# Kernel optimization log

Hardware: AMD Instinct MI355X
Metric: run time of the kernel (lower is better)

## Reference

```python
import jax, jax.numpy as jnp
import numpy as np

MP1, NX, P, HT, HE = 524288, 32768, 128, 128, 64


def setup_inputs() -> dict:
    key = jax.random.key(0)
    ks = jax.random.split(key, 12)
    w = lambda k, shape, fan_in: jax.random.normal(k, shape, jnp.float32) / np.sqrt(fan_in).astype(np.float32)
    a = jax.random.normal(ks[0], (MP1,), jnp.float32)
    x = jax.random.uniform(ks[1], (NX,), jnp.float32)
    t = jax.random.uniform(ks[2], (), jnp.float32)
    # DeepONet-style operator net: branch Linear(Mp1 -> p), trunk MLP (x,t) -> p
    Wb = w(ks[3], (P, MP1), MP1); bb = jnp.zeros((P,), jnp.float32)
    Wt1 = w(ks[4], (HT, 2), 2); bt1 = jnp.zeros((HT,), jnp.float32)
    Wt2 = w(ks[5], (HT, HT), HT); bt2 = jnp.zeros((HT,), jnp.float32)
    Wt3 = w(ks[6], (P, HT), HT); bt3 = jnp.zeros((P,), jnp.float32)
    # EnergyNet F(y,z): tiny smooth MLP R^2 -> R (needs 3rd-order derivatives)
    We1 = w(ks[7], (HE, 2), 2); be1 = jnp.zeros((HE,), jnp.float32)
    We2 = w(ks[8], (HE, HE), HE); be2 = jnp.zeros((HE,), jnp.float32)
    We3 = w(ks[9], (1, HE), HE); be3 = jnp.zeros((1,), jnp.float32)
    return dict(a=a, x=x, t=t, Wb=Wb, bb=bb, Wt1=Wt1, bt1=bt1, Wt2=Wt2, bt2=bt2,
                Wt3=Wt3, bt3=bt3, We1=We1, be1=be1, We2=We2, be2=be2, We3=We3, be3=be3)


def reference(a, x, t, Wb, bb, Wt1, bt1, Wt2, bt2, Wt3, bt3, We1, be1, We2, be2, We3, be3):
    # branch encoding of the input function a: (P,)
    b = Wb @ a + bb

    def u_fn(xi):  # scalar x -> scalar u(x, t)
        h = jnp.tanh(Wt1 @ jnp.stack([xi, t]) + bt1)
        h = jnp.tanh(Wt2 @ h + bt2)
        return jnp.dot(b, Wt3 @ h + bt3)

    def F(y, z):  # EnergyNet: scalar (y, z) -> scalar
        h = jnp.tanh(We1 @ jnp.stack([y, z]) + be1)
        h = jnp.tanh(We2 @ h + be2)
        return (We3 @ h + be3)[0]

    # u and its spatial derivatives, vmapped over the Nx grid points
    u = jax.vmap(u_fn)(x)
    u_x = jax.vmap(jax.grad(u_fn))(x)
    u_xx = jax.vmap(jax.grad(jax.grad(u_fn)))(x)
    u_xxx = jax.vmap(jax.grad(jax.grad(jax.grad(u_fn))))(x)

    # all needed partials of F(y, z), exactly as in the original module
    F_y = jax.grad(F)
    F_yz = jax.vmap(jax.grad(F_y, 1))(u, u_x)
    F_yy, F_yyz = jax.vmap(jax.value_and_grad(jax.grad(F_y), 1))(u, u_x)
    F_zz, (F_yzz, F_zzz) = jax.vmap(jax.value_and_grad(jax.grad(jax.grad(F, 1), 1), (0, 1)))(u, u_x)

    F_yx = F_yy * u_x + F_yz * u_xx
    F_zxx = (F_yz * u_xx + F_zz * u_xxx + F_yyz * u_x ** 2
             + 2.0 * F_yzz * u_x * u_xx + F_zzz * u_xx ** 2)
    return (-F_yx + F_zxx).reshape(x.shape[0])
```

## Files before the change

kernel.cpp:

```cpp
#include <hip/hip_runtime.h>
#include <cmath>

#define MP1 524288
#define NXP 32768

typedef float vfloat4 __attribute__((ext_vector_type(4)));

#define PART_   0
#define CVEC_   4096
#define UCONST_ 4224
#define WT2T_   8192
#define WE2T_   24576

__device__ __forceinline__ float tanh_fast(float x) {
    x = fminf(20.f, fmaxf(-20.f, x));
    float t = exp2f(x * 2.8853900817779268f);
    return (t - 1.f) * __builtin_amdgcn_rcpf(t + 1.f);
}

__global__ __launch_bounds__(256) void gemv_k(const float* __restrict__ Wb,
                                              const float* __restrict__ a,
                                              float* __restrict__ ws) {
    const int row = blockIdx.x;
    const int chunk = blockIdx.y;
    const int t = threadIdx.x;
    size_t base = (size_t)row * MP1 + (size_t)chunk * 16384;
    const vfloat4* W4 = (const vfloat4*)(Wb + base);
    const float4* A4 = (const float4*)(a + (size_t)chunk * 16384);
    float sum = 0.0f;
#pragma unroll
    for (int it = 0; it < 16; ++it) {
        vfloat4 w = __builtin_nontemporal_load(&W4[t + it * 256]);
        float4 av = A4[t + it * 256];
        sum += w[0] * av.x + w[1] * av.y + w[2] * av.z + w[3] * av.w;
    }
#pragma unroll
    for (int off = 32; off > 0; off >>= 1) sum += __shfl_down(sum, off, 64);
    __shared__ float red[4];
    int wid = t >> 6;
    if ((t & 63) == 0) red[wid] = sum;
    __syncthreads();
    if (t == 0) ws[PART_ + row * 32 + chunk] = red[0] + red[1] + red[2] + red[3];
}

__global__ __launch_bounds__(256) void prep_k(const float* __restrict__ bb,
                                              const float* __restrict__ Wt2,
                                              const float* __restrict__ We2,
                                              const float* __restrict__ Wt3,
                                              const float* __restrict__ bt3,
                                              float* __restrict__ ws) {
    const int tid = threadIdx.x;
    if (blockIdx.x == 0) {
        __shared__ float sh[128];
        __shared__ float red[2];
        if (tid < 128) {
            float b = bb[tid];
            const float* part = ws + PART_ + tid * 32;
#pragma unroll
            for (int c = 0; c < 32; ++c) b += part[c];
            sh[tid] = b;
        }
        __syncthreads();
        if (tid < 128) {
            float cv = 0.f;
            for (int j = 0; j < 128; ++j) cv = fmaf(sh[j], Wt3[j * 128 + tid], cv);
            ws[CVEC_ + tid] = cv;
            float p = sh[tid] * bt3[tid];
#pragma unroll
            for (int off = 32; off > 0; off >>= 1) p += __shfl_down(p, off, 64);
            if ((tid & 63) == 0) red[tid >> 6] = p;
        }
        __syncthreads();
        if (tid == 0) ws[UCONST_] = red[0] + red[1];
    } else {
        int idx = (blockIdx.x - 1) * 256 + tid;
        int j = idx >> 7, k = idx & 127;
        ws[WT2T_ + k * 128 + j] = Wt2[idx];
        if (idx < 4096) {
            int m = idx >> 6, i2 = idx & 63;
            ws[WE2T_ + i2 * 64 + m] = We2[idx];
        }
    }
}

#define SW_WT1 0
#define SW_BT1 256
#define SW_BT2 384
#define SW_CVEC 512
#define SW_WE1X 640
#define SW_BE1 1152
#define SW_BE2 1216
#define SW_WE3 1280
#define UREDP 1344
#define H1V_ 1600
#define FREDP (H1V_ + 4096)
#define SCR_ 9792
#define LDSF 13888

__global__ __launch_bounds__(512, 4) void point_k(const float* __restrict__ x,
                                                  const float* __restrict__ tptr,
                                                  const float* __restrict__ Wt1,
                                                  const float* __restrict__ bt1,
                                                  const float* __restrict__ bt2,
                                                  const float* __restrict__ We1,
                                                  const float* __restrict__ be1,
                                                  const float* __restrict__ be2,
                                                  const float* __restrict__ We3,
                                                  const float* __restrict__ ws,
                                                  float* __restrict__ out) {
    __shared__ __align__(16) float lds[LDSF];
    const int tid = threadIdx.x;
    const int p = tid & 63;
    const int slice = __builtin_amdgcn_readfirstlane(tid >> 6);
    const int i = blockIdx.x * 64 + p;
    const float xi = x[i];
    const float tt = tptr[0];
    const float u_const = ws[UCONST_];

    if (tid < 256) lds[SW_WT1 + tid] = Wt1[tid];
    else if (tid < 384) lds[SW_BT1 + tid - 256] = bt1[tid - 256];
    else lds[SW_BT2 + tid - 384] = bt2[tid - 384];
    if (tid < 128) lds[SW_CVEC + tid] = ws[CVEC_ + tid];
    else if (tid < 192) lds[SW_BE1 + tid - 128] = be1[tid - 128];
    else if (tid < 256) lds[SW_BE2 + tid - 192] = be2[tid - 192];
    else if (tid < 320) lds[SW_WE3 + tid - 256] = We3[tid - 256];
    else if (tid < 384) {
        int ii = tid - 320;
        float w0 = We1[2 * ii], w1 = We1[2 * ii + 1];
        float w00 = w0 * w0, w01 = w0 * w1, w11 = w1 * w1;
        float* X = lds + SW_WE1X + ii * 8;
        X[0] = w0; X[1] = w1; X[2] = w00; X[3] = w01; X[4] = w11;
        X[5] = w00 * w1; X[6] = w01 * w1; X[7] = w11 * w1;
    }
    __syncthreads();

#pragma unroll
    for (int q = 0; q < 16; ++q) {
        int k = slice * 16 + q;
        float z = fmaf(lds[SW_WT1 + 2 * k], xi,
                       fmaf(lds[SW_WT1 + 2 * k + 1], tt, lds[SW_BT1 + k]));
        lds[H1V_ + k * 64 + p] = tanh_fast(z);
    }

    float a0[16], a1[16], a2[16], a3[16];
#pragma unroll
    for (int jj = 0; jj < 16; ++jj) { a0[jj] = 0.f; a1[jj] = 0.f; a2[jj] = 0.f; a3[jj] = 0.f; }
    for (int c = 0; c < 4; ++c) {
        __syncthreads();
        {
            const float4* src = (const float4*)(ws + WT2T_ + c * 4096);
            float4* dst = (float4*)(lds + SCR_);
            dst[tid] = src[tid];
            dst[tid + 512] = src[tid + 512];
        }
        __syncthreads();
#pragma unroll 1
        for (int kl = 0; kl < 32; ++kl) {
            int k = c * 32 + kl;
            float v = lds[H1V_ + k * 64 + p];
            float w = lds[SW_WT1 + 2 * k];
            float s = fmaf(-v, v, 1.f);
            float t2 = v * s;
            float m = fmaf(-3.f, s, 2.f);
            float sm = s * m;
            float w2 = w * w, w3 = w2 * w;
            float d1 = s * w;
            float d2 = t2 * w2;
            float d3 = sm * w3;
            const float4* wr = (const float4*)(lds + SCR_ + kl * 128 + slice * 16);
            float4 wv0 = wr[0], wv1 = wr[1], wv2 = wr[2], wv3 = wr[3];
            const float wf[16] = {wv0.x, wv0.y, wv0.z, wv0.w, wv1.x, wv1.y, wv1.z, wv1.w,
                                  wv2.x, wv2.y, wv2.z, wv2.w, wv3.x, wv3.y, wv3.z, wv3.w};
#pragma unroll
            for (int jj = 0; jj < 16; ++jj) {
                float wjk = wf[jj];
                a0[jj] = fmaf(wjk, v, a0[jj]);
                a1[jj] = fmaf(wjk, d1, a1[jj]);
                a2[jj] = fmaf(wjk, d2, a2[jj]);
                a3[jj] = fmaf(wjk, d3, a3[jj]);
            }
        }
    }
    float u0 = 0.f, u1 = 0.f, u2 = 0.f, u3 = 0.f;
#pragma unroll
    for (int jj = 0; jj < 16; ++jj) {
        int j = slice * 16 + jj;
        float z0 = a0[jj] + lds[SW_BT2 + j];
        float z1 = a1[jj], z2 = -2.f * a2[jj], z3 = 2.f * a3[jj];
        float v = tanh_fast(z0);
        float s = 1.f - v * v;
        float f2 = -2.f * v * s;
        float f3 = 2.f * s * (2.f * v * v - s);
        float cj = lds[SW_CVEC + j];
        u0 = fmaf(cj, v, u0);
        u1 = fmaf(cj, s * z1, u1);
        u2 = fmaf(cj, f2 * z1 * z1 + s * z2, u2);
        u3 = fmaf(cj, f3 * z1 * z1 * z1 + 3.f * f2 * z1 * z2 + s * z3, u3);
    }
    __syncthreads();
    lds[SCR_ + 0 * 512 + slice * 64 + p] = u0;
    lds[SCR_ + 1 * 512 + slice * 64 + p] = u1;
    lds[SCR_ + 2 * 512 + slice * 64 + p] = u2;
    lds[SCR_ + 3 * 512 + slice * 64 + p] = u3;
    __syncthreads();

    if (tid < 64) {
        float r0 = u_const, r1 = 0.f, r2 = 0.f, r3 = 0.f;
#pragma unroll
        for (int s = 0; s < 8; ++s) {
            r0 += lds[SCR_ + 0 * 512 + s * 64 + tid];
            r1 += lds[SCR_ + 1 * 512 + s * 64 + tid];
            r2 += lds[SCR_ + 2 * 512 + s * 64 + tid];
            r3 += lds[SCR_ + 3 * 512 + s * 64 + tid];
        }
        lds[UREDP + 0 * 64 + tid] = r0;
        lds[UREDP + 1 * 64 + tid] = r1;
        lds[UREDP + 2 * 64 + tid] = r2;
        lds[UREDP + 3 * 64 + tid] = r3;
    }
    __syncthreads();

    {
        const float4* src = (const float4*)(ws + WE2T_);
        float4* dst = (float4*)(lds + SCR_);
        dst[tid] = src[tid];
        dst[tid + 512] = src[tid + 512];
    }
    const float y = lds[UREDP + 0 * 64 + p];
    const float z = lds[UREDP + 1 * 64 + p];
#pragma unroll
    for (int q = 0; q < 8; ++q) {
        int ii = slice * 8 + q;
        float g = fmaf(lds[SW_WE1X + ii * 8], y,
                       fmaf(lds[SW_WE1X + ii * 8 + 1], z, lds[SW_BE1 + ii]));
        lds[H1V_ + ii * 64 + p] = tanh_fast(g);
    }
    __syncthreads();

    {
        float A0[8], A1[8], A2[8], A3[8], A4[8], A5[8], A6[8], A7[8], A8[8];
#pragma unroll
        for (int mm = 0; mm < 8; ++mm) {
            A0[mm] = 0.f; A1[mm] = 0.f; A2[mm] = 0.f; A3[mm] = 0.f; A4[mm] = 0.f;
            A5[mm] = 0.f; A6[mm] = 0.f; A7[mm] = 0.f; A8[mm] = 0.f;
        }
#pragma unroll 1
        for (int ii = 0; ii < 64; ++ii) {
            float v = lds[H1V_ + ii * 64 + p];
            const float4* xw = (const float4*)(lds + SW_WE1X + ii * 8);
            float4 xa = xw[0], xb = xw[1];
            float s = fmaf(-v, v, 1.f);
            float t2 = v * s;
            float m = fmaf(-3.f, s, 2.f);
            float sm = s * m;
            float j1 = s * xa.x, j2 = s * xa.y;
            float j3 = t2 * xa.z, j4 = t2 * xa.w, j5 = t2 * xb.x;
            float j6 = sm * xb.y, j7 = sm * xb.z, j8 = sm * xb.w;
            const float4* wr = (const float4*)(lds + SCR_ + ii * 64 + slice * 8);
            float4 wv0 = wr[0], wv1 = wr[1];
            const float wf[8] = {wv0.x, wv0.y, wv0.z, wv0.w, wv1.x, wv1.y, wv1.z, wv1.w};
#pragma unroll
            for (int mm = 0; mm < 8; ++mm) {
                float wmi = wf[mm];
                A0[mm] = fmaf(wmi, v,  A0[mm]);
                A1[mm] = fmaf(wmi, j1, A1[mm]);
                A2[mm] = fmaf(wmi, j2, A2[mm]);
                A3[mm] = fmaf(wmi, j3, A3[mm]);
                A4[mm] = fmaf(wmi, j4, A4[mm]);
                A5[mm] = fmaf(wmi, j5, A5[mm]);
                A6[mm] = fmaf(wmi, j6, A6[mm]);
                A7[mm] = fmaf(wmi, j7, A7[mm]);
                A8[mm] = fmaf(wmi, j8, A8[mm]);
            }
        }
        float Fyy = 0.f, Fyz = 0.f, Fzz = 0.f, Fyyz = 0.f, Fyzz = 0.f, Fzzz = 0.f;
#pragma unroll
        for (int mm = 0; mm < 8; ++mm) {
            int m = slice * 8 + mm;
            float G0 = A0[mm] + lds[SW_BE2 + m];
            float v = tanh_fast(G0);
            float s = 1.f - v * v;
            float f2 = -2.f * v * s;
            float f3 = 2.f * s * (2.f * v * v - s);
            float Gy = A1[mm], Gz = A2[mm];
            float Gyy = -2.f * A3[mm], Gyz = -2.f * A4[mm], Gzz = -2.f * A5[mm];
            float Gyyz = 2.f * A6[mm], Gyzz = 2.f * A7[mm], Gzzz = 2.f * A8[mm];
            float Hyy = f2 * Gy * Gy + s * Gyy;
            float Hyz = f2 * Gy * Gz + s * Gyz;
            float Hzz = f2 * Gz * Gz + s * Gzz;
            float Hyyz = f3 * Gy * Gy * Gz + f2 * (Gyy * Gz + 2.f * Gyz * Gy) + s * Gyyz;
            float Hyzz = f3 * Gy * Gz * Gz + f2 * (2.f * Gyz * Gz + Gzz * Gy) + s * Gyzz;
            float Hzzz = f3 * Gz * Gz * Gz + 3.f * f2 * Gzz * Gz + s * Gzzz;
            float w3 = lds[SW_WE3 + m];
            Fyy  = fmaf(w3, Hyy,  Fyy);
            Fyz  = fmaf(w3, Hyz,  Fyz);
            Fzz  = fmaf(w3, Hzz,  Fzz);
            Fyyz = fmaf(w3, Hyyz, Fyyz);
            Fyzz = fmaf(w3, Hyzz, Fyzz);
            Fzzz = fmaf(w3, Hzzz, Fzzz);
        }
        lds[FREDP + 0 * 512 + slice * 64 + p] = Fyy;
        lds[FREDP + 1 * 512 + slice * 64 + p] = Fyz;
        lds[FREDP + 2 * 512 + slice * 64 + p] = Fzz;
        lds[FREDP + 3 * 512 + slice * 64 + p] = Fyyz;
        lds[FREDP + 4 * 512 + slice * 64 + p] = Fyzz;
        lds[FREDP + 5 * 512 + slice * 64 + p] = Fzzz;
    }
    __syncthreads();

    if (tid < 64) {
        float F[6] = {0.f, 0.f, 0.f, 0.f, 0.f, 0.f};
#pragma unroll
        for (int s = 0; s < 8; ++s) {
#pragma unroll
            for (int q = 0; q < 6; ++q) F[q] += lds[FREDP + q * 512 + s * 64 + tid];
        }
        float u1r = lds[UREDP + 1 * 64 + tid];
        float u2r = lds[UREDP + 2 * 64 + tid];
        float u3r = lds[UREDP + 3 * 64 + tid];
        float F_yx  = F[0] * u1r + F[1] * u2r;
        float F_zxx = F[1] * u2r + F[2] * u3r + F[3] * u1r * u1r
                    + 2.f * F[4] * u1r * u2r + F[5] * u2r * u2r;
        out[blockIdx.x * 64 + tid] = F_zxx - F_yx;
    }
}

extern "C" void kernel_launch(void* const* d_in, const int* in_sizes, int n_in,
                              void* d_out, int out_size, void* d_ws, size_t ws_size,
                              hipStream_t stream) {
    const float* a   = (const float*)d_in[0];
    const float* x   = (const float*)d_in[1];
    const float* t   = (const float*)d_in[2];
    const float* Wb  = (const float*)d_in[3];
    const float* bb  = (const float*)d_in[4];
    const float* Wt1 = (const float*)d_in[5];
    const float* bt1 = (const float*)d_in[6];
    const float* Wt2 = (const float*)d_in[7];
    const float* bt2 = (const float*)d_in[8];
    const float* Wt3 = (const float*)d_in[9];
    const float* bt3 = (const float*)d_in[10];
    const float* We1 = (const float*)d_in[11];
    const float* be1 = (const float*)d_in[12];
    const float* We2 = (const float*)d_in[13];
    const float* be2 = (const float*)d_in[14];
    const float* We3 = (const float*)d_in[15];

    float* ws = (float*)d_ws;
    float* out = (float*)d_out;

    gemv_k<<<dim3(128, 32), 256, 0, stream>>>(Wb, a, ws);
    prep_k<<<65, 256, 0, stream>>>(bb, Wt2, We2, Wt3, bt3, ws);
    point_k<<<NXP / 64, 512, 0, stream>>>(x, t, Wt1, bt1, bt2, We1, be1, be2, We3,
                                          ws, out);
}
```

Baseline: 460.8 us.

## Fold prep kernel into gemv and point kernels, recompute branch vector per block

Removes the separate prep kernel launch. The weight transposes, including a new transposed Wt3, now run in extra gemv grid rows. Each point block reduces the gemv partials itself and computes the Wt3-projected c vector and the constant term redundantly. The Wt2 staging loop now uses two larger chunks instead of four, and precomputed powers of the trunk weight are read from a small LDS table. This trades one launch and a serial single-block dependency for redundant per-block work and larger LDS use, which may lower occupancy.

```diff
diff --git a/kernel.cpp b/kernel.cpp
--- a/kernel.cpp
+++ b/kernel.cpp
@@ -7,10 +7,9 @@
 typedef float vfloat4 __attribute__((ext_vector_type(4)));
 
 #define PART_   0
-#define CVEC_   4096
-#define UCONST_ 4224
 #define WT2T_   8192
 #define WE2T_   24576
+#define WT3T_   28672
 
 __device__ __forceinline__ float tanh_fast(float x) {
     x = fminf(20.f, fmaxf(-20.f, x));
@@ -20,67 +19,50 @@
 
 __global__ __launch_bounds__(256) void gemv_k(const float* __restrict__ Wb,
                                               const float* __restrict__ a,
+                                              const float* __restrict__ Wt2,
+                                              const float* __restrict__ We2,
+                                              const float* __restrict__ Wt3,
                                               float* __restrict__ ws) {
+    const int y = blockIdx.y;
+    const int tid = threadIdx.x;
+    if (y >= 32) {
+        int idx = blockIdx.x * 256 + tid;
+        if (y == 32) {
+            if (idx < 16384) {
+                int j = idx >> 7, k = idx & 127;
+                ws[WT2T_ + k * 128 + j] = Wt2[idx];
+            } else if (idx < 20480) {
+                int e = idx - 16384;
+                int m = e >> 6, i2 = e & 63;
+                ws[WE2T_ + i2 * 64 + m] = We2[e];
+            }
+        } else {
+            if (idx < 16384) {
+                int j = idx >> 7, k = idx & 127;
+                ws[WT3T_ + k * 128 + j] = Wt3[idx];
+            }
+        }
+        return;
+    }
     const int row = blockIdx.x;
-    const int chunk = blockIdx.y;
-    const int t = threadIdx.x;
+    const int chunk = y;
     size_t base = (size_t)row * MP1 + (size_t)chunk * 16384;
     const vfloat4* W4 = (const vfloat4*)(Wb + base);
     const float4* A4 = (const float4*)(a + (size_t)chunk * 16384);
     float sum = 0.0f;
 #pragma unroll
     for (int it = 0; it < 16; ++it) {
-        vfloat4 w = __builtin_nontemporal_load(&W4[t + it * 256]);
-        float4 av = A4[t + it * 256];
+        vfloat4 w = __builtin_nontemporal_load(&W4[tid + it * 256]);
+        float4 av = A4[tid + it * 256];
         sum += w[0] * av.x + w[1] * av.y + w[2] * av.z + w[3] * av.w;
     }
 #pragma unroll
     for (int off = 32; off > 0; off >>= 1) sum += __shfl_down(sum, off, 64);
     __shared__ float red[4];
-    int wid = t >> 6;
-    if ((t & 63) == 0) red[wid] = sum;
-    __syncthreads();
-    if (t == 0) ws[PART_ + row * 32 + chunk] = red[0] + red[1] + red[2] + red[3];
-}
-
-__global__ __launch_bounds__(256) void prep_k(const float* __restrict__ bb,
-                                              const float* __restrict__ Wt2,
-                                              const float* __restrict__ We2,
-                                              const float* __restrict__ Wt3,
-                                              const float* __restrict__ bt3,
-                                              float* __restrict__ ws) {
-    const int tid = threadIdx.x;
-    if (blockIdx.x == 0) {
-        __shared__ float sh[128];
-        __shared__ float red[2];
-        if (tid < 128) {
-            float b = bb[tid];
-            const float* part = ws + PART_ + tid * 32;
-#pragma unroll
-            for (int c = 0; c < 32; ++c) b += part[c];
-            sh[tid] = b;
-        }
-        __syncthreads();
-        if (tid < 128) {
-            float cv = 0.f;
-            for (int j = 0; j < 128; ++j) cv = fmaf(sh[j], Wt3[j * 128 + tid], cv);
-            ws[CVEC_ + tid] = cv;
-            float p = sh[tid] * bt3[tid];
-#pragma unroll
-            for (int off = 32; off > 0; off >>= 1) p += __shfl_down(p, off, 64);
-            if ((tid & 63) == 0) red[tid >> 6] = p;
-        }
-        __syncthreads();
-        if (tid == 0) ws[UCONST_] = red[0] + red[1];
-    } else {
-        int idx = (blockIdx.x - 1) * 256 + tid;
-        int j = idx >> 7, k = idx & 127;
-        ws[WT2T_ + k * 128 + j] = Wt2[idx];
-        if (idx < 4096) {
-            int m = idx >> 6, i2 = idx & 63;
-            ws[WE2T_ + i2 * 64 + m] = We2[idx];
-        }
-    }
+    int wid = tid >> 6;
+    if ((tid & 63) == 0) red[wid] = sum;
+    __syncthreads();
+    if (tid == 0) ws[PART_ + row * 32 + chunk] = red[0] + red[1] + red[2] + red[3];
 }
 
 #define SW_WT1 0
@@ -91,11 +73,14 @@
 #define SW_BE1 1152
 #define SW_BE2 1216
 #define SW_WE3 1280
-#define UREDP 1344
-#define H1V_ 1600
+#define SW_B 1344
+#define WTAB 1472
+#define REDU 1984
+#define UREDP 2000
+#define H1V_ 2256
 #define FREDP (H1V_ + 4096)
-#define SCR_ 9792
-#define LDSF 13888
+#define SCR_ 10448
+#define LDSF 18640
 
 __global__ __launch_bounds__(512, 4) void point_k(const float* __restrict__ x,
                                                   const float* __restrict__ tptr,
@@ -106,6 +91,8 @@
                                                   const float* __restrict__ be1,
                                                   const float* __restrict__ be2,
                                                   const float* __restrict__ We3,
+                                                  const float* __restrict__ bb,
+                                                  const float* __restrict__ bt3,
                                                   const float* __restrict__ ws,
                                                   float* __restrict__ out) {
     __shared__ __align__(16) float lds[LDSF];
@@ -115,13 +102,15 @@
     const int i = blockIdx.x * 64 + p;
     const float xi = x[i];
     const float tt = tptr[0];
-    const float u_const = ws[UCONST_];
 
     if (tid < 256) lds[SW_WT1 + tid] = Wt1[tid];
     else if (tid < 384) lds[SW_BT1 + tid - 256] = bt1[tid - 256];
     else lds[SW_BT2 + tid - 384] = bt2[tid - 384];
-    if (tid < 128) lds[SW_CVEC + tid] = ws[CVEC_ + tid];
-    else if (tid < 192) lds[SW_BE1 + tid - 128] = be1[tid - 128];
+    if (tid < 128) {
+        float w0 = Wt1[2 * tid];
+        float* T = lds + WTAB + tid * 4;
+        T[0] = w0; T[1] = w0 * w0; T[2] = w0 * w0 * w0; T[3] = 0.f;
+    } else if (tid < 192) lds[SW_BE1 + tid - 128] = be1[tid - 128];
     else if (tid < 256) lds[SW_BE2 + tid - 192] = be2[tid - 192];
     else if (tid < 320) lds[SW_WE3 + tid - 256] = We3[tid - 256];
     else if (tid < 384) {
@@ -131,6 +120,16 @@
         float* X = lds + SW_WE1X + ii * 8;
         X[0] = w0; X[1] = w1; X[2] = w00; X[3] = w01; X[4] = w11;
         X[5] = w00 * w1; X[6] = w01 * w1; X[7] = w11 * w1;
+    } else {
+        int j = tid - 384;
+        const float4* P4 = (const float4*)(ws + PART_ + j * 32);
+        float b = bb[j];
+#pragma unroll
+        for (int q = 0; q < 8; ++q) {
+            float4 v4 = P4[q];
+            b += v4.x; b += v4.y; b += v4.z; b += v4.w;
+        }
+        lds[SW_B + j] = b;
     }
     __syncthreads();
 
@@ -141,32 +140,51 @@
                        fmaf(lds[SW_WT1 + 2 * k + 1], tt, lds[SW_BT1 + k]));
         lds[H1V_ + k * 64 + p] = tanh_fast(z);
     }
+    if (tid < 128) {
+        float cv = 0.f;
+        const float4* W4 = (const float4*)(ws + WT3T_ + tid * 128);
+#pragma unroll 4
+        for (int q = 0; q < 32; ++q) {
+            float4 wv = W4[q];
+            cv = fmaf(lds[SW_B + 4 * q + 0], wv.x, cv);
+            cv = fmaf(lds[SW_B + 4 * q + 1], wv.y, cv);
+            cv = fmaf(lds[SW_B + 4 * q + 2], wv.z, cv);
+            cv = fmaf(lds[SW_B + 4 * q + 3], wv.w, cv);
+        }
+        lds[SW_CVEC + tid] = cv;
+        float pk_ = lds[SW_B + tid] * bt3[tid];
+#pragma unroll
+        for (int off = 32; off > 0; off >>= 1) pk_ += __shfl_down(pk_, off, 64);
+        if ((tid & 63) == 0) lds[REDU + (tid >> 6)] = pk_;
+    }
 
     float a0[16], a1[16], a2[16], a3[16];
 #pragma unroll
     for (int jj = 0; jj < 16; ++jj) { a0[jj] = 0.f; a1[jj] = 0.f; a2[jj] = 0.f; a3[jj] = 0.f; }
-    for (int c = 0; c < 4; ++c) {
+    for (int c = 0; c < 2; ++c) {
         __syncthreads();
         {
-            const float4* src = (const float4*)(ws + WT2T_ + c * 4096);
+            const float4* src = (const float4*)(ws + WT2T_ + c * 8192);
             float4* dst = (float4*)(lds + SCR_);
             dst[tid] = src[tid];
             dst[tid + 512] = src[tid + 512];
+            dst[tid + 1024] = src[tid + 1024];
+            dst[tid + 1536] = src[tid + 1536];
         }
         __syncthreads();
 #pragma unroll 1
-        for (int kl = 0; kl < 32; ++kl) {
-            int k = c * 32 + kl;
+        for (int kl = 0; kl < 64; ++kl) {
+            int k = c * 64 + kl;
             float v = lds[H1V_ + k * 64 + p];
-            float w = lds[SW_WT1 + 2 * k];
+            const float4* wtp = (const float4*)(lds + WTAB + k * 4);
+            float4 wt = wtp[0];
             float s = fmaf(-v, v, 1.f);
             float t2 = v * s;
             float m = fmaf(-3.f, s, 2.f);
             float sm = s * m;
-            float w2 = w * w, w3 = w2 * w;
-            float d1 = s * w;
-            float d2 = t2 * w2;
-            float d3 = sm * w3;
+            float d1 = s * wt.x;
+            float d2 = t2 * wt.y;
+            float d3 = sm * wt.z;
             const float4* wr = (const float4*)(lds + SCR_ + kl * 128 + slice * 16);
             float4 wv0 = wr[0], wv1 = wr[1], wv2 = wr[2], wv3 = wr[3];
             const float wf[16] = {wv0.x, wv0.y, wv0.z, wv0.w, wv1.x, wv1.y, wv1.z, wv1.w,
@@ -205,7 +223,8 @@
     __syncthreads();
 
     if (tid < 64) {
-        float r0 = u_const, r1 = 0.f, r2 = 0.f, r3 = 0.f;
+        float r0 = lds[REDU] + lds[REDU + 1];
+        float r1 = 0.f, r2 = 0.f, r3 = 0.f;
 #pragma unroll
         for (int s = 0; s < 8; ++s) {
             r0 += lds[SCR_ + 0 * 512 + s * 64 + tid];
@@ -348,8 +367,7 @@
     float* ws = (float*)d_ws;
     float* out = (float*)d_out;
 
-    gemv_k<<<dim3(128, 32), 256, 0, stream>>>(Wb, a, ws);
-    prep_k<<<65, 256, 0, stream>>>(bb, Wt2, We2, Wt3, bt3, ws);
+    gemv_k<<<dim3(128, 34), 256, 0, stream>>>(Wb, a, Wt2, We2, Wt3, ws);
     point_k<<<NXP / 64, 512, 0, stream>>>(x, t, Wt1, bt1, bt2, We1, be1, be2, We3,
-                                          ws, out);
+                                          bb, bt3, ws, out);
 }
```

After: 458.7 us. Within noise of the previous version (-0.5%).
